# Kernel tuning notes

Measured on AMD Instinct MI355X. Metric: run time of the kernel, lower is better.

## Reference

```python
import jax, jax.numpy as jnp
import numpy as np

B, S, D = 4, 4096, 1024
DFF = 4 * D
ACTIVE = 1024  # ceil(S * 0.25)


def setup_inputs() -> dict:
    key = jax.random.key(0)
    ks = jax.random.split(key, 4)
    x = jax.random.normal(ks[0], (B, S, D), dtype=jnp.float32)
    rw = jax.random.normal(ks[1], (D,), dtype=jnp.float32) * 0.02
    rb = jnp.zeros((1,), dtype=jnp.float32)
    w1 = jax.random.normal(ks[2], (D, DFF), dtype=jnp.float32) * 0.02
    b1 = jnp.zeros((DFF,), dtype=jnp.float32)
    w2 = jax.random.normal(ks[3], (DFF, D), dtype=jnp.float32) * 0.02
    b2 = jnp.zeros((D,), dtype=jnp.float32)
    return {"x": x, "rw": rw, "rb": rb, "w1": w1, "b1": b1,
            "w2": w2, "b2": b2, "active_tokens": ACTIVE}


def reference(x, rw, rb, w1, b1, w2, b2, active_tokens):
    b, s, d = x.shape
    # router: Linear(n_embd, 1) -> [B, S] scores
    scores = jnp.einsum('bsd,d->bs', x, rw) + rb[0]
    # top-k tokens per batch row
    _, idx = jax.lax.top_k(scores, active_tokens)          # [B, K] int32
    sel = jnp.take_along_axis(x, idx[..., None], axis=1)   # [B, K, D]
    # dense MLP on selected tokens (exact GELU as in torch nn.GELU)
    h = jax.nn.gelu(jnp.einsum('bkd,df->bkf', sel, w1) + b1, approximate=False)
    out = jnp.einsum('bkf,fd->bkd', h, w2) + b2            # [B, K, D]
    # sigmoid gate from router scores of selected tokens
    gates = jax.nn.sigmoid(jnp.take_along_axis(scores, idx, axis=1))  # [B, K]
    out = out * gates[..., None]
    # scatter back into zeros at selected positions
    flat_idx = (idx + jnp.arange(b, dtype=idx.dtype)[:, None] * s).reshape(-1)
    flat_out = jnp.zeros((b * s, d), dtype=out.dtype)
    flat_out = flat_out.at[flat_idx].set(out.reshape(-1, d))
    return flat_out.reshape(b, s, d)
```

## Files before the change

### kernel.cpp

```cpp
#include <hip/hip_runtime.h>
#include <hip/hip_bf16.h>
#include <cstdint>
#include <cstddef>

#define Bz 4
#define Sz 4096
#define Dz 1024
#define DFFz 4096
#define KACT 1024

typedef __bf16 bf16;
typedef __attribute__((ext_vector_type(8))) __bf16 bf16x8;
typedef __attribute__((ext_vector_type(4))) __bf16 bf16x4;
typedef __attribute__((ext_vector_type(4))) float f32x4;

__device__ __forceinline__ void async16(const void* g, void* l) {
  __builtin_amdgcn_global_load_lds(
      (const __attribute__((address_space(1))) void*)g,
      (__attribute__((address_space(3))) void*)l, 16, 0, 0);
}

__global__ void router_k(const float* __restrict__ x, const float* __restrict__ rw,
                         const float* __restrict__ rb, float* __restrict__ scores,
                         float4* __restrict__ out4) {
  int row = blockIdx.x * 4 + (threadIdx.x >> 6);
  int lane = threadIdx.x & 63;
  const float4* xr = (const float4*)(x + (size_t)row * Dz);
  const float4* wr = (const float4*)rw;
  float acc = 0.f;
#pragma unroll
  for (int i = 0; i < 4; ++i) {
    float4 a = xr[lane + i * 64];
    float4 w = wr[lane + i * 64];
    acc += a.x * w.x + a.y * w.y + a.z * w.z + a.w * w.w;
  }
#pragma unroll
  for (int d = 32; d; d >>= 1) acc += __shfl_down(acc, d, 64);
  if (lane == 0) scores[row] = acc + rb[0];
  float4* o = out4 + (size_t)blockIdx.x * 4 * (Dz / 4);
  const float4 z = make_float4(0.f, 0.f, 0.f, 0.f);
#pragma unroll
  for (int i = 0; i < 4; ++i) o[threadIdx.x + i * 256] = z;
}

__global__ void transpose_cvt(const float* __restrict__ in, bf16* __restrict__ out,
                              int R, int C) {
  __shared__ float t[32][33];
  int c0 = blockIdx.x * 32, r0 = blockIdx.y * 32;
  int tx = threadIdx.x, ty = threadIdx.y;
#pragma unroll
  for (int i = 0; i < 32; i += 8) t[ty + i][tx] = in[(size_t)(r0 + ty + i) * C + c0 + tx];
  __syncthreads();
#pragma unroll
  for (int i = 0; i < 32; i += 8)
    out[(size_t)(c0 + ty + i) * R + r0 + tx] = (bf16)t[tx][ty + i];
}

__global__ __launch_bounds__(256) void select_gather_k(
    const float* __restrict__ x, const float* __restrict__ scores,
    int* __restrict__ sel_idx, float* __restrict__ gates, bf16* __restrict__ Xsel) {
  int b = blockIdx.x >> 8;
  int s0 = (blockIdx.x & 255) * 16;
  __shared__ float sc[Sz];
  __shared__ int red[16][4];
  __shared__ int rk[16];
  const int tid = threadIdx.x;
  const int wave = tid >> 6, lane = tid & 63;
  const float* srow = scores + (size_t)b * Sz;
#pragma unroll
  for (int i = 0; i < 4; ++i)
    ((float4*)sc)[tid + i * 256] = ((const float4*)srow)[tid + i * 256];
  __syncthreads();
  float mine[16];
#pragma unroll
  for (int j = 0; j < 16; ++j) mine[j] = sc[s0 + j];
  int cnt[16] = {};
  for (int t = tid; t < Sz; t += 256) {
    float o = sc[t];
#pragma unroll
    for (int j = 0; j < 16; ++j)
      cnt[j] += (o > mine[j]) || (o == mine[j] && t < s0 + j);
  }
#pragma unroll
  for (int j = 0; j < 16; ++j) {
    int c = cnt[j];
#pragma unroll
    for (int d = 32; d; d >>= 1) c += __shfl_down(c, d, 64);
    if (lane == 0) red[j][wave] = c;
  }
  __syncthreads();
  if (tid < 16) {
    int rank = red[tid][0] + red[tid][1] + red[tid][2] + red[tid][3];
    rk[tid] = rank;
    if (rank < KACT) {
      int m = b * KACT + rank;
      sel_idx[m] = s0 + tid;
      gates[m] = 1.f / (1.f + expf(-sc[s0 + tid]));
    }
  }
  __syncthreads();
#pragma unroll
  for (int j = 0; j < 16; ++j) {
    int rank = rk[j];
    if (rank >= KACT) continue;
    int m = b * KACT + rank;
    float4 v = ((const float4*)(x + ((size_t)b * Sz + s0 + j) * Dz))[tid];
    bf16x4 o = {(bf16)v.x, (bf16)v.y, (bf16)v.z, (bf16)v.w};
    ((bf16x4*)(Xsel + (size_t)m * Dz))[tid] = o;
  }
}

#define PROD_ISSUE(buf, k0)                                                    \
  _Pragma("unroll")                                                            \
  for (int h = 0; h < 2; ++h) {                                                \
    async16(Ag + (k0) + h * 32, &As[buf][h * 4096 + q * 8]);                   \
    async16(Ag + (size_t)64 * K + (k0) + h * 32, &As[buf][h * 4096 + 2048 + q * 8]); \
    async16(Bg + (k0) + h * 32, &Bs[buf][h * 4096 + q * 8]);                   \
    async16(Bg + (size_t)64 * K + (k0) + h * 32, &Bs[buf][h * 4096 + 2048 + q * 8]); \
  }

#define PIPE_GEMM_BODY(KV, KOFF, NITER)                                        \
  __shared__ __align__(16) bf16 As[2][2 * 128 * 32];            \
  __shared__ __align__(16) bf16 Bs[2][2 * 128 * 32];                           \
  constexpr int K = (KV);                                                      \
  const int tid = threadIdx.x;                                                 \
  const int wave = tid >> 6, lane = tid & 63;                                  \
  const int quad = lane >> 4, l16 = lane & 15;                                 \
  const int m0 = blockIdx.y * 128, n0 = blockIdx.x * 128;                      \
  const int wm = (wave >> 1) * 64, wn = (wave & 1) * 64;                       \
  const int q = tid & 255;                                                     \
  const bf16* Ag = A + (size_t)(m0 + (q >> 2)) * K + (KOFF) + (q & 3) * 8;     \
  const bf16* Bg = Bt + (size_t)(n0 + (q >> 2)) * K + (KOFF) + (q & 3) * 8;    \
  f32x4 acc[4][4] = {};                                                        \
  if (wave >= 4) { PROD_ISSUE(0, 0) }                                          \
  __syncthreads();                                                             \
  for (int it = 0; it < (NITER); ++it) {                                       \
    if (wave >= 4) {                                                           \
      if (it + 1 < (NITER)) { PROD_ISSUE((it + 1) & 1, (it + 1) * 64) }        \
    } else {                                                                   \
      const int cur = it & 1;                                                  \
      _Pragma("unroll")                                                        \
      for (int h = 0; h < 2; ++h) {                                            \
        bf16x8 af[4], bfr[4];                                                  \
        _Pragma("unroll")                                                      \
        for (int i = 0; i < 4; ++i) {                                          \
          af[i] = *(const bf16x8*)&As[cur][h * 4096 + (wm + i * 16 + l16) * 32 + quad * 8]; \
          bfr[i] = *(const bf16x8*)&Bs[cur][h * 4096 + (wn + i * 16 + l16) * 32 + quad * 8]; \
        }                                                                      \
        _Pragma("unroll")                                                      \
        for (int mi = 0; mi < 4; ++mi)                                         \
          _Pragma("unroll")                                                    \
          for (int ni = 0; ni < 4; ++ni)                                       \
            acc[mi][ni] = __builtin_amdgcn_mfma_f32_16x16x32_bf16(af[mi], bfr[ni], acc[mi][ni], 0, 0, 0); \
      }                                                                        \
    }                                                                          \
    __syncthreads();                                                           \
  }

__global__ __launch_bounds__(512, 4) void gemm1_k(const bf16* __restrict__ A,
                                                  const bf16* __restrict__ Bt,
                                                  const float* __restrict__ bias,
                                                  bf16* __restrict__ H) {
  constexpr int N = DFFz;
  PIPE_GEMM_BODY(Dz, 0, Dz / 64)
  if (wave < 4) {
#pragma unroll
    for (int mi = 0; mi < 4; ++mi) {
      int mbase = m0 + wm + mi * 16 + quad * 4;
#pragma unroll
      for (int ni = 0; ni < 4; ++ni) {
        int n = n0 + wn + ni * 16 + l16;
        float bn = bias[n];
#pragma unroll
        for (int r = 0; r < 4; ++r) {
          float z = acc[mi][ni][r] + bn;
          float g = 0.5f * z * (1.f + erff(z * 0.70710678118654752f));
          H[(size_t)(mbase + r) * N + n] = (bf16)g;
        }
      }
    }
  }
}

__global__ __launch_bounds__(512, 4) void gemm2_k(const bf16* __restrict__ A,
                                                  const bf16* __restrict__ Bt,
                                                  bf16* __restrict__ P) {
  PIPE_GEMM_BODY(DFFz, blockIdx.z * 2048, 2048 / 64)
  if (wave < 4) {
    bf16* Pc = P + (size_t)blockIdx.z * Bz * KACT * Dz;
#pragma unroll
    for (int mi = 0; mi < 4; ++mi) {
      int mbase = m0 + wm + mi * 16 + quad * 4;
#pragma unroll
      for (int ni = 0; ni < 4; ++ni) {
        int n = n0 + wn + ni * 16 + l16;
#pragma unroll
        for (int r = 0; r < 4; ++r)
          Pc[(size_t)(mbase + r) * Dz + n] = (bf16)acc[mi][ni][r];
      }
    }
  }
}

__global__ __launch_bounds__(256) void reduce_k(const bf16* __restrict__ P,
                                                const float* __restrict__ bias,
                                                const int* __restrict__ sel_idx,
                                                const float* __restrict__ gates,
                                                float* __restrict__ out) {
  int m = blockIdx.x;
  int b = m >> 10;
  int s = sel_idx[m];
  float gt = gates[m];
  int tid = threadIdx.x;
  const bf16x4* p0 = (const bf16x4*)(P + (size_t)m * Dz);
  const bf16x4* p1 = (const bf16x4*)(P + (size_t)Bz * KACT * Dz + (size_t)m * Dz);
  const float4* bv = (const float4*)bias;
  float4* orow = (float4*)(out + ((size_t)b * Sz + s) * Dz);
  bf16x4 a = p0[tid], c = p1[tid];
  float4 bb = bv[tid];
  float4 o;
  o.x = ((float)a[0] + (float)c[0] + bb.x) * gt;
  o.y = ((float)a[1] + (float)c[1] + bb.y) * gt;
  o.z = ((float)a[2] + (float)c[2] + bb.z) * gt;
  o.w = ((float)a[3] + (float)c[3] + bb.w) * gt;
  orow[tid] = o;
}

extern "C" void kernel_launch(void* const* d_in, const int* in_sizes, int n_in,
                              void* d_out, int out_size, void* d_ws, size_t ws_size,
                              hipStream_t stream) {
  (void)in_sizes; (void)n_in; (void)out_size; (void)ws_size;
  const float* x  = (const float*)d_in[0];
  const float* rw = (const float*)d_in[1];
  const float* rb = (const float*)d_in[2];
  const float* w1 = (const float*)d_in[3];
  const float* b1 = (const float*)d_in[4];
  const float* w2 = (const float*)d_in[5];
  const float* b2 = (const float*)d_in[6];
  float* out = (float*)d_out;

  char* ws = (char*)d_ws;
  float* scores = (float*)ws;  ws += (size_t)Bz * Sz * 4;
  int*   sel_idx = (int*)ws;   ws += (size_t)Bz * KACT * 4;
  float* gates = (float*)ws;   ws += (size_t)Bz * KACT * 4;
  bf16*  w2T = (bf16*)ws;      ws += (size_t)Dz * DFFz * 2;
  bf16*  H = (bf16*)ws;        ws += (size_t)Bz * KACT * DFFz * 2;
  bf16*  w1T = (bf16*)ws;      ws += (size_t)DFFz * Dz * 2;
  bf16*  Xsel = (bf16*)ws;     ws += (size_t)Bz * KACT * Dz * 2;
  bf16*  P = w1T;

  router_k<<<(Bz * Sz) / 4, 256, 0, stream>>>(x, rw, rb, scores, (float4*)out);
  transpose_cvt<<<dim3(DFFz / 32, Dz / 32), dim3(32, 8), 0, stream>>>(w1, w1T, Dz, DFFz);
  transpose_cvt<<<dim3(Dz / 32, DFFz / 32), dim3(32, 8), 0, stream>>>(w2, w2T, DFFz, Dz);
  select_gather_k<<<Bz * (Sz / 16), 256, 0, stream>>>(x, scores, sel_idx, gates, Xsel);
  gemm1_k<<<dim3(DFFz / 128, (Bz * KACT) / 128), 512, 0, stream>>>(Xsel, w1T, b1, H);
  gemm2_k<<<dim3(Dz / 128, (Bz * KACT) / 128, 2), 512, 0, stream>>>(H, w2T, P);
  reduce_k<<<Bz * KACT, 256, 0, stream>>>(P, b2, sel_idx, gates, out);
}
```

Before: 293.0 us.

## Fuse router and weight transposes into one prep kernel; halve GEMM K-step

Merges the router/zero-fill kernel and both weight transpose-convert kernels into one launch, dispatching on block index, which removes two launches and lets the independent work overlap. It also shrinks the GEMM pipeline's K-step from 64 to 32, halving shared-memory buffers so more blocks fit per CU. The cost is twice as many iterations, each with a barrier and less MFMA work between syncs.

```diff
diff --git a/kernel.cpp b/kernel.cpp
--- a/kernel.cpp
+++ b/kernel.cpp
@@ -20,40 +20,55 @@
       (__attribute__((address_space(3))) void*)l, 16, 0, 0);
 }
 
-__global__ void router_k(const float* __restrict__ x, const float* __restrict__ rw,
-                         const float* __restrict__ rb, float* __restrict__ scores,
-                         float4* __restrict__ out4) {
-  int row = blockIdx.x * 4 + (threadIdx.x >> 6);
-  int lane = threadIdx.x & 63;
-  const float4* xr = (const float4*)(x + (size_t)row * Dz);
-  const float4* wr = (const float4*)rw;
-  float acc = 0.f;
-#pragma unroll
-  for (int i = 0; i < 4; ++i) {
-    float4 a = xr[lane + i * 64];
-    float4 w = wr[lane + i * 64];
-    acc += a.x * w.x + a.y * w.y + a.z * w.z + a.w * w.w;
-  }
-#pragma unroll
-  for (int d = 32; d; d >>= 1) acc += __shfl_down(acc, d, 64);
-  if (lane == 0) scores[row] = acc + rb[0];
-  float4* o = out4 + (size_t)blockIdx.x * 4 * (Dz / 4);
-  const float4 z = make_float4(0.f, 0.f, 0.f, 0.f);
-#pragma unroll
-  for (int i = 0; i < 4; ++i) o[threadIdx.x + i * 256] = z;
-}
-
-__global__ void transpose_cvt(const float* __restrict__ in, bf16* __restrict__ out,
-                              int R, int C) {
+__global__ __launch_bounds__(256) void prep_k(const float* __restrict__ x,
+                                              const float* __restrict__ rw,
+                                              const float* __restrict__ rb,
+                                              float* __restrict__ scores,
+                                              float4* __restrict__ out4,
+                                              const float* __restrict__ w1,
+                                              bf16* __restrict__ w1T,
+                                              const float* __restrict__ w2,
+                                              bf16* __restrict__ w2T) {
   __shared__ float t[32][33];
-  int c0 = blockIdx.x * 32, r0 = blockIdx.y * 32;
-  int tx = threadIdx.x, ty = threadIdx.y;
-#pragma unroll
-  for (int i = 0; i < 32; i += 8) t[ty + i][tx] = in[(size_t)(r0 + ty + i) * C + c0 + tx];
-  __syncthreads();
-#pragma unroll
-  for (int i = 0; i < 32; i += 8)
-    out[(size_t)(c0 + ty + i) * R + r0 + tx] = (bf16)t[tx][ty + i];
+  const int bid = blockIdx.x;
+  const int tid = threadIdx.x;
+  if (bid < 4096) {
+    int row = bid * 4 + (tid >> 6);
+    int lane = tid & 63;
+    const float4* xr = (const float4*)(x + (size_t)row * Dz);
+    const float4* wr = (const float4*)rw;
+    float acc = 0.f;
+#pragma unroll
+    for (int i = 0; i < 4; ++i) {
+      float4 a = xr[lane + i * 64];
+      float4 w = wr[lane + i * 64];
+      acc += a.x * w.x + a.y * w.y + a.z * w.z + a.w * w.w;
+    }
+#pragma unroll
+    for (int d = 32; d; d >>= 1) acc += __shfl_down(acc, d, 64);
+    if (lane == 0) scores[row] = acc + rb[0];
+    float4* o = out4 + (size_t)bid * 4 * (Dz / 4);
+    const float4 z = make_float4(0.f, 0.f, 0.f, 0.f);
+#pragma unroll
+    for (int i = 0; i < 4; ++i) o[tid + i * 256] = z;
+  } else {
+    const float* in; bf16* outp; int R, C, bx, by;
+    if (bid < 8192) {
+      in = w1; outp = w1T; R = Dz; C = DFFz;
+      bx = (bid - 4096) & 127; by = (bid - 4096) >> 7;
+    } else {
+      in = w2; outp = w2T; R = DFFz; C = Dz;
+      bx = (bid - 8192) & 31; by = (bid - 8192) >> 5;
+    }
+    int c0 = bx * 32, r0 = by * 32;
+    int tx = tid & 31, ty = tid >> 5;
+#pragma unroll
+    for (int i = 0; i < 32; i += 8) t[ty + i][tx] = in[(size_t)(r0 + ty + i) * C + c0 + tx];
+    __syncthreads();
+#pragma unroll
+    for (int i = 0; i < 32; i += 8)
+      outp[(size_t)(c0 + ty + i) * R + r0 + tx] = (bf16)t[tx][ty + i];
+  }
 }
 
 __global__ __launch_bounds__(256) void select_gather_k(
@@ -111,17 +126,14 @@
 }
 
 #define PROD_ISSUE(buf, k0)                                                    \
-  _Pragma("unroll")                                                            \
-  for (int h = 0; h < 2; ++h) {                                                \
-    async16(Ag + (k0) + h * 32, &As[buf][h * 4096 + q * 8]);                   \
-    async16(Ag + (size_t)64 * K + (k0) + h * 32, &As[buf][h * 4096 + 2048 + q * 8]); \
-    async16(Bg + (k0) + h * 32, &Bs[buf][h * 4096 + q * 8]);                   \
-    async16(Bg + (size_t)64 * K + (k0) + h * 32, &Bs[buf][h * 4096 + 2048 + q * 8]); \
-  }
+  async16(Ag + (k0), &As[buf][q * 8]);                                         \
+  async16(Ag + (size_t)64 * K + (k0), &As[buf][2048 + q * 8]);                 \
+  async16(Bg + (k0), &Bs[buf][q * 8]);                                         \
+  async16(Bg + (size_t)64 * K + (k0), &Bs[buf][2048 + q * 8]);
 
 #define PIPE_GEMM_BODY(KV, KOFF, NITER)                                        \
-  __shared__ __align__(16) bf16 As[2][2 * 128 * 32];            \
-  __shared__ __align__(16) bf16 Bs[2][2 * 128 * 32];                           \
+  __shared__ __align__(16) bf16 As[2][128 * 32];                 \
+  __shared__ __align__(16) bf16 Bs[2][128 * 32];                               \
   constexpr int K = (KV);                                                      \
   const int tid = threadIdx.x;                                                 \
   const int wave = tid >> 6, lane = tid & 63;                                  \
@@ -136,23 +148,20 @@
   __syncthreads();                                                             \
   for (int it = 0; it < (NITER); ++it) {                                       \
     if (wave >= 4) {                                                           \
-      if (it + 1 < (NITER)) { PROD_ISSUE((it + 1) & 1, (it + 1) * 64) }        \
+      if (it + 1 < (NITER)) { PROD_ISSUE((it + 1) & 1, (it + 1) * 32) }        \
     } else {                                                                   \
       const int cur = it & 1;                                                  \
+      bf16x8 af[4], bfr[4];                                                    \
       _Pragma("unroll")                                                        \
-      for (int h = 0; h < 2; ++h) {                                            \
-        bf16x8 af[4], bfr[4];                                                  \
+      for (int i = 0; i < 4; ++i) {                                            \
+        af[i] = *(const bf16x8*)&As[cur][(wm + i * 16 + l16) * 32 + quad * 8]; \
+        bfr[i] = *(const bf16x8*)&Bs[cur][(wn + i * 16 + l16) * 32 + quad * 8]; \
+      }                                                                        \
+      _Pragma("unroll")                                                        \
+      for (int mi = 0; mi < 4; ++mi)                                           \
         _Pragma("unroll")                                                      \
-        for (int i = 0; i < 4; ++i) {                                          \
-          af[i] = *(const bf16x8*)&As[cur][h * 4096 + (wm + i * 16 + l16) * 32 + quad * 8]; \
-          bfr[i] = *(const bf16x8*)&Bs[cur][h * 4096 + (wn + i * 16 + l16) * 32 + quad * 8]; \
-        }                                                                      \
-        _Pragma("unroll")                                                      \
-        for (int mi = 0; mi < 4; ++mi)                                         \
-          _Pragma("unroll")                                                    \
-          for (int ni = 0; ni < 4; ++ni)                                       \
-            acc[mi][ni] = __builtin_amdgcn_mfma_f32_16x16x32_bf16(af[mi], bfr[ni], acc[mi][ni], 0, 0, 0); \
-      }                                                                        \
+        for (int ni = 0; ni < 4; ++ni)                                         \
+          acc[mi][ni] = __builtin_amdgcn_mfma_f32_16x16x32_bf16(af[mi], bfr[ni], acc[mi][ni], 0, 0, 0); \
     }                                                                          \
     __syncthreads();                                                           \
   }
@@ -162,7 +171,7 @@
                                                   const float* __restrict__ bias,
                                                   bf16* __restrict__ H) {
   constexpr int N = DFFz;
-  PIPE_GEMM_BODY(Dz, 0, Dz / 64)
+  PIPE_GEMM_BODY(Dz, 0, Dz / 32)
   if (wave < 4) {
 #pragma unroll
     for (int mi = 0; mi < 4; ++mi) {
@@ -185,7 +194,7 @@
 __global__ __launch_bounds__(512, 4) void gemm2_k(const bf16* __restrict__ A,
                                                   const bf16* __restrict__ Bt,
                                                   bf16* __restrict__ P) {
-  PIPE_GEMM_BODY(DFFz, blockIdx.z * 2048, 2048 / 64)
+  PIPE_GEMM_BODY(DFFz, blockIdx.z * 2048, 2048 / 32)
   if (wave < 4) {
     bf16* Pc = P + (size_t)blockIdx.z * Bz * KACT * Dz;
 #pragma unroll
@@ -249,9 +258,7 @@
   bf16*  Xsel = (bf16*)ws;     ws += (size_t)Bz * KACT * Dz * 2;
   bf16*  P = w1T;
 
-  router_k<<<(Bz * Sz) / 4, 256, 0, stream>>>(x, rw, rb, scores, (float4*)out);
-  transpose_cvt<<<dim3(DFFz / 32, Dz / 32), dim3(32, 8), 0, stream>>>(w1, w1T, Dz, DFFz);
-  transpose_cvt<<<dim3(Dz / 32, DFFz / 32), dim3(32, 8), 0, stream>>>(w2, w2T, DFFz, Dz);
+  prep_k<<<3 * 4096, 256, 0, stream>>>(x, rw, rb, scores, (float4*)out, w1, w1T, w2, w2T);
   select_gather_k<<<Bz * (Sz / 16), 256, 0, stream>>>(x, scores, sel_idx, gates, Xsel);
   gemm1_k<<<dim3(DFFz / 128, (Bz * KACT) / 128), 512, 0, stream>>>(Xsel, w1T, b1, H);
   gemm2_k<<<dim3(Dz / 128, (Bz * KACT) / 128, 2), 512, 0, stream>>>(H, w2T, P);
```

Result: no change. 291.9 us (-0.4%).
